# Performance work log

Measured on AMD Instinct MI355X. Metric: run time of the kernel, lower is better.

Reference implementation:

```python
import jax, jax.numpy as jnp
import numpy as np

M_DIM, Z_DIM, C = 256, 128, 32
N, L = 512, 384


def setup_inputs() -> dict:
    key = jax.random.key(0)
    ks = jax.random.split(key, 9)
    s = 1.0 / np.sqrt(M_DIM)
    return {
        "m": jax.random.normal(ks[0], (N, L, M_DIM), dtype=jnp.float32),
        "ln_gamma": jnp.ones((M_DIM,), jnp.float32),
        "ln_beta": jnp.zeros((M_DIM,), jnp.float32),
        "w1": jax.random.normal(ks[1], (M_DIM, C), jnp.float32) * s,
        "b1": jnp.zeros((C,), jnp.float32),
        "w2": jax.random.normal(ks[2], (M_DIM, C), jnp.float32) * s,
        "b2": jnp.zeros((C,), jnp.float32),
        "w3": jax.random.normal(ks[3], (C * C, Z_DIM), jnp.float32) * (1.0 / np.sqrt(C * C)),
        "b3": jnp.zeros((Z_DIM,), jnp.float32),
    }


def _layernorm(x, gamma, beta, eps=1e-5):
    mu = jnp.mean(x, axis=-1, keepdims=True)
    var = jnp.mean(jnp.square(x - mu), axis=-1, keepdims=True)
    return (x - mu) * jax.lax.rsqrt(var + eps) * gamma + beta


def reference(m, ln_gamma, ln_beta, w1, b1, w2, b2, w3, b3):
    n = m.shape[0]
    o = _layernorm(m, ln_gamma, ln_beta)          # (N, L, D)
    a = o @ w2 + b2                                # (N, L, C)  linear2
    b = o @ w1 + b1                                # (N, L, C)  linear1
    # mean over N of outer products: reassociated as a single contraction over n
    op = jnp.einsum('nia,njb->ijab', a, b) / n     # (L, L, C, C)
    ll = op.shape[0]
    z = op.reshape(ll, ll, -1) @ w3 + b3           # (L, L, Z)
    return z
```

## Files before the change

### kernel.cpp

```cpp
#include <hip/hip_runtime.h>
#include <hip/hip_bf16.h>
#include <stdint.h>

#define L_DIM 384
#define MD    256
#define CC    32
#define ZD    128
#define NB    512
#define K2    1024
#define MROWS 12288

typedef __attribute__((ext_vector_type(4)))  float f32x4;
typedef __attribute__((ext_vector_type(8)))  short bf16x8;

typedef __attribute__((address_space(1))) unsigned char* gcp;
typedef __attribute__((address_space(3))) unsigned char* lcp;

#define SBAR()  __builtin_amdgcn_s_barrier()
#define VMW(n)  asm volatile("s_waitcnt vmcnt(" #n ")" ::: "memory")
#define PRIO1() __builtin_amdgcn_s_setprio(1)
#define PRIO0() __builtin_amdgcn_s_setprio(0)

__device__ __forceinline__ unsigned short f2bf(float x) {
    union { float f; unsigned u; } v; v.f = x;
    unsigned r = v.u + 0x7fffu + ((v.u >> 16) & 1u);
    return (unsigned short)(r >> 16);
}

__device__ __forceinline__ uint2 pack4(unsigned short a, unsigned short b,
                                       unsigned short c, unsigned short d) {
    uint2 r; r.x = (unsigned)a | ((unsigned)b << 16);
    r.y = (unsigned)c | ((unsigned)d << 16); return r;
}

__global__ __launch_bounds__(256) void prep_kernel(
    const float* __restrict__ w1, const float* __restrict__ w2,
    const float* __restrict__ w3,
    unsigned short* __restrict__ w3frag, unsigned short* __restrict__ wfrag)
{
    int idx = blockIdx.x * 256 + threadIdx.x;
    if (idx < 131072) {
        int e = idx & 7, lane = (idx >> 3) & 63, zg = (idx >> 9) & 7, ks = idx >> 12;
        int k2p = ks * 32 + ((lane >> 4) << 3) + e;
        int wrow = (k2p & 31) * 32 + (k2p >> 5);
        int z  = zg * 16 + (lane & 15);
        w3frag[idx] = f2bf(w3[(size_t)wrow * ZD + z]);
    } else {
        int j = idx - 131072;
        int e = j & 7, lane = (j >> 3) & 63, nf = (j >> 9) & 3, ks = j >> 11;
        int c = nf * 16 + (lane & 15);
        int d = ks * 32 + ((lane >> 4) << 3) + e;
        float v = (c < CC) ? w2[d * CC + c] : w1[d * CC + (c - CC)];
        wfrag[j] = f2bf(v);
    }
}

__global__ __launch_bounds__(256, 4) void ln_proj_kernel(
    const float* __restrict__ mm, const float* __restrict__ gamma, const float* __restrict__ beta,
    const unsigned short* __restrict__ wfrag,
    const float* __restrict__ b1, const float* __restrict__ b2,
    unsigned short* __restrict__ At, unsigned short* __restrict__ Bt)
{
    __shared__ alignas(16) char o_b[32768];

    const int tid = threadIdx.x, wv = tid >> 6, lane = tid & 63;
    const int l0 = blockIdx.y * 2;
    const int n0 = blockIdx.x * 32;

    const int l_loc = wv >> 1;
    const int nbase = (wv & 1) << 4;
    const int l_g = l0 + l_loc;
    f32x4 g4 = *(const f32x4*)(gamma + lane * 4);
    f32x4 e4 = *(const f32x4*)(beta + lane * 4);

    #pragma unroll 4
    for (int r = 0; r < 16; ++r) {
        int row_loc = wv * 16 + r;
        int n_g = n0 + nbase + r;
        const float* src = mm + ((size_t)n_g * L_DIM + l_g) * MD + lane * 4;
        f32x4 x = *(const f32x4*)src;
        float s  = x[0] + x[1] + x[2] + x[3];
        float s2 = x[0]*x[0] + x[1]*x[1] + x[2]*x[2] + x[3]*x[3];
        #pragma unroll
        for (int off = 32; off > 0; off >>= 1) {
            s  += __shfl_xor(s,  off);
            s2 += __shfl_xor(s2, off);
        }
        float mu  = s * (1.0f / MD);
        float var = s2 * (1.0f / MD) - mu * mu;
        float rs  = rsqrtf(var + 1e-5f);
        unsigned short o0 = f2bf((x[0] - mu) * rs * g4[0] + e4[0]);
        unsigned short o1 = f2bf((x[1] - mu) * rs * g4[1] + e4[1]);
        unsigned short o2 = f2bf((x[2] - mu) * rs * g4[2] + e4[2]);
        unsigned short o3 = f2bf((x[3] - mu) * rs * g4[3] + e4[3]);
        *(uint2*)(o_b + row_loc * 512 + ((lane * 8) ^ ((row_loc & 7) << 4))) = pack4(o0, o1, o2, o3);
    }

    f32x4 acc[4] = {{0,0,0,0},{0,0,0,0},{0,0,0,0},{0,0,0,0}};
    const int lrow = lane & 15;
    const int kq16 = (lane >> 4) << 4;
    const int arow = wv * 16 + lrow;
    #pragma unroll
    for (int ks = 0; ks < 8; ++ks) {
        bf16x8 a = *(const bf16x8*)(o_b + arow * 512 + ((ks * 64 + kq16) ^ ((arow & 7) << 4)));
        #pragma unroll
        for (int nf = 0; nf < 4; ++nf) {
            bf16x8 b = *(const bf16x8*)(wfrag + (size_t)((ks * 4 + nf) * 64 + lane) * 8);
            acc[nf] = __builtin_amdgcn_mfma_f32_16x16x32_bf16(a, b, acc[nf], 0, 0, 0);
        }
    }

    const int rr0 = wv * 16 + ((lane >> 4) << 2);
    const int n_gw = n0 + (rr0 & 31);
    const int l_gw = l0 + (rr0 >> 5);
    #pragma unroll
    for (int nf = 0; nf < 4; ++nf) {
        int c = nf * 16 + lrow;
        float bias = (c < CC) ? b2[c] : b1[c - CC];
        unsigned short ob0 = f2bf(acc[nf][0] + bias);
        unsigned short ob1 = f2bf(acc[nf][1] + bias);
        unsigned short ob2 = f2bf(acc[nf][2] + bias);
        unsigned short ob3 = f2bf(acc[nf][3] + bias);
        unsigned short* dst = ((c < CC) ? At : Bt) + (size_t)(l_gw * CC + (c & 31)) * NB + n_gw;
        *(uint2*)dst = pack4(ob0, ob1, ob2, ob3);
    }
}

__global__ __launch_bounds__(512, 4) void opm_kernel(
    const unsigned short* __restrict__ At, const unsigned short* __restrict__ Bt,
    const unsigned short* __restrict__ w3frag, const float* __restrict__ b3,
    float* __restrict__ Z)
{
    __shared__ alignas(128) char smem[73728];
    const int tid = threadIdx.x, wv = tid >> 6, lane = tid & 63;

    const int lin = blockIdx.x;
    const int xcd = lin & 7, c = lin >> 3;
    const int i0 = (xcd * 12 + (c % 12)) * 128;
    const int j0 = (c / 12) * 256;

    const int lrow = lane & 15;
    const int wrB = (wv >> 2) * 64, wcB = (wv & 3) * 64;

    const int f0 = wv * 3;
    const int s_row = lane >> 2;
    const int s_kof = ((lane & 3) ^ (s_row & 3)) << 3;

    auto stage = [&](int t) {
        const int buf = t % 3;
        #pragma unroll
        for (int q = 0; q < 3; ++q) {
            int f = f0 + q;
            const unsigned short* g;
            char* l;
            if (f < 8) {
                g = At + (size_t)(i0 + f * 16 + s_row) * NB + t * 32 + s_kof;
                l = smem + buf * 8192 + f * 1024;
            } else {
                g = Bt + (size_t)(j0 + (f - 8) * 16 + s_row) * NB + t * 32 + s_kof;
                l = smem + 24576 + buf * 16384 + (f - 8) * 1024;
            }
            __builtin_amdgcn_global_load_lds((gcp)g, (lcp)l, 16, 0, 0);
        }
    };

    f32x4 acc[4][4] = {};
    const int rpos = ((lane >> 4) ^ (lane & 3)) << 4;

    auto TILE = [&](int t) {
        const char* ab = smem + (t % 3) * 8192;
        const char* bb = smem + 24576 + (t % 3) * 16384;
        bf16x8 av[4], bv[4];
        #pragma unroll
        for (int mf = 0; mf < 4; ++mf)
            av[mf] = *(const bf16x8*)(ab + (wrB + mf * 16 + lrow) * 64 + rpos);
        #pragma unroll
        for (int nf = 0; nf < 4; ++nf)
            bv[nf] = *(const bf16x8*)(bb + (wcB + nf * 16 + lrow) * 64 + rpos);
        PRIO1();
        #pragma unroll
        for (int mf = 0; mf < 4; ++mf)
            #pragma unroll
            for (int nf = 0; nf < 4; ++nf)
                acc[mf][nf] = __builtin_amdgcn_mfma_f32_16x16x32_bf16(
                    av[mf], bv[nf], acc[mf][nf], 0, 0, 0);
        PRIO0();
    };

    stage(0); stage(1);
    VMW(3);
    SBAR();

    #pragma unroll
    for (int t = 0; t < 16; ++t) {
        if (t < 14) stage(t + 2);
        TILE(t);
        if (t < 14)      { VMW(3); }
        else if (t == 14){ VMW(0); }
        SBAR();
    }

    char* const opb = smem;
    const int pf  = wv & 1;
    const int zgb = (wv >> 1) * 2;
    const int row0 = pf * 16 + lrow;
    const int lq = lane >> 4;

    auto ldW = [&](int ks, int zg) -> bf16x8 {
        return *(const bf16x8*)(w3frag + (size_t)((ks * 8 + zg) * 64 + lane) * 8);
    };
    auto ldP = [&](int row, int ks) -> bf16x8 {
        int g = ks * 4 + lq;
        int b = g >> 2, jj = g & 3;
        int inner = (b * 64 + jj * 16) ^ (((b >> 1) & 7) << 4) ^ ((row & 7) << 4);
        return *(const bf16x8*)(opb + row * 2048 + inner);
    };

    bf16x8 wA0 = ldW(0, zgb), wA1 = ldW(0, zgb + 1);

    const float scale = 1.0f / (float)NB;
    #pragma unroll
    for (int mf = 0; mf < 4; ++mf) {
        #pragma unroll
        for (int nf = 0; nf < 4; ++nf) {
            int col = wcB + nf * 16 + lrow;
            int bcol = col & 31;
            int row = wrB + mf * 16 + ((lane >> 4) << 2);
            int pl = ((row >> 5) << 3) | (col >> 5);
            int a0e = row & 31;
            int inner = (bcol * 64 + a0e * 2) ^ (((bcol >> 1) & 7) << 4) ^ ((pl & 7) << 4);
            *(uint2*)(opb + pl * 2048 + inner) =
                pack4(f2bf(acc[mf][nf][0] * scale), f2bf(acc[mf][nf][1] * scale),
                      f2bf(acc[mf][nf][2] * scale), f2bf(acc[mf][nf][3] * scale));
        }
    }
    __syncthreads();

    f32x4 acc2[2] = {};
    bf16x8 pA = ldP(row0, 0);
    for (int ks = 0; ks < 32; ++ks) {
        bf16x8 wN0 = {}, wN1 = {}, pN = {};
        if (ks + 1 < 32) {
            wN0 = ldW(ks + 1, zgb); wN1 = ldW(ks + 1, zgb + 1);
            pN  = ldP(row0, ks + 1);
        }
        PRIO1();
        acc2[0] = __builtin_amdgcn_mfma_f32_16x16x32_bf16(pA, wA0, acc2[0], 0, 0, 0);
        acc2[1] = __builtin_amdgcn_mfma_f32_16x16x32_bf16(pA, wA1, acc2[1], 0, 0, 0);
        PRIO0();
        wA0 = wN0; wA1 = wN1; pA = pN;
    }

    const int pq = (lane >> 4) << 2;
    #pragma unroll
    for (int zi = 0; zi < 2; ++zi) {
        int zc = (zgb + zi) * 16 + lrow;
        float bias = b3[zc];
        #pragma unroll
        for (int rr = 0; rr < 4; ++rr) {
            int pl = pf * 16 + pq + rr;
            int ii = (i0 >> 5) + (pl >> 3);
            int jj = (j0 >> 5) + (pl & 7);
            Z[((size_t)ii * L_DIM + jj) * ZD + zc] = acc2[zi][rr] + bias;
        }
    }
}

extern "C" void kernel_launch(void* const* d_in, const int* in_sizes, int n_in,
                              void* d_out, int out_size, void* d_ws, size_t ws_size,
                              hipStream_t stream)
{
    const float* mm    = (const float*)d_in[0];
    const float* gamma = (const float*)d_in[1];
    const float* beta  = (const float*)d_in[2];
    const float* w1    = (const float*)d_in[3];
    const float* b1    = (const float*)d_in[4];
    const float* w2    = (const float*)d_in[5];
    const float* b2    = (const float*)d_in[6];
    const float* w3    = (const float*)d_in[7];
    const float* b3    = (const float*)d_in[8];

    unsigned short* At     = (unsigned short*)d_ws;
    unsigned short* Bt     = At + (size_t)MROWS * NB;
    unsigned short* w3frag = Bt + (size_t)MROWS * NB;
    unsigned short* wfrag  = w3frag + 131072;

    prep_kernel<<<576, 256, 0, stream>>>(w1, w2, w3, w3frag, wfrag);
    ln_proj_kernel<<<dim3(16, 192), 256, 0, stream>>>(mm, gamma, beta, wfrag, b1, b2, At, Bt);
    opm_kernel<<<4608, 512, 0, stream>>>(At, Bt, w3frag, b3, (float*)d_out);
}
```

Measured before the change: 278.8 us.

## Switch OPM GEMM to 32x32 MFMA with B fragments prepacked in global memory

The first kernel now writes the B projection in an MFMA-fragment-ordered layout, so the outer-product kernel can load B operands straight from global memory into registers through a 4-deep register prefetch instead of staging them in LDS. Only A is staged, in 128-wide K chunks that are double-buffered, which cuts the number of barriers from 16 to a few and shrinks LDS use. The inner product uses 32x32x16 MFMAs with 2x2 accumulator tiles instead of 4x4 tiles of 16x16x32, and the epilogue scatter into the op buffer is adapted to the new accumulator layout. The risks are higher register pressure from the prefetched B fragments and more global traffic for B, since each wave reads its B fragments from cache directly.

```diff
diff --git a/kernel.cpp b/kernel.cpp
--- a/kernel.cpp
+++ b/kernel.cpp
@@ -11,6 +11,7 @@
 #define MROWS 12288
 
 typedef __attribute__((ext_vector_type(4)))  float f32x4;
+typedef __attribute__((ext_vector_type(16))) float f32x16;
 typedef __attribute__((ext_vector_type(8)))  short bf16x8;
 
 typedef __attribute__((address_space(1))) unsigned char* gcp;
@@ -117,12 +118,16 @@
     for (int nf = 0; nf < 4; ++nf) {
         int c = nf * 16 + lrow;
         float bias = (c < CC) ? b2[c] : b1[c - CC];
-        unsigned short ob0 = f2bf(acc[nf][0] + bias);
-        unsigned short ob1 = f2bf(acc[nf][1] + bias);
-        unsigned short ob2 = f2bf(acc[nf][2] + bias);
-        unsigned short ob3 = f2bf(acc[nf][3] + bias);
-        unsigned short* dst = ((c < CC) ? At : Bt) + (size_t)(l_gw * CC + (c & 31)) * NB + n_gw;
-        *(uint2*)dst = pack4(ob0, ob1, ob2, ob3);
+        uint2 pk = pack4(f2bf(acc[nf][0] + bias), f2bf(acc[nf][1] + bias),
+                         f2bf(acc[nf][2] + bias), f2bf(acc[nf][3] + bias));
+        if (c < CC) {
+            *(uint2*)(At + (size_t)(l_gw * CC + c) * NB + n_gw) = pk;
+        } else {
+            int c31 = c - CC;
+            size_t addr = (((size_t)l_gw * 32 + (n_gw >> 4)) * 64
+                           + c31 + (((n_gw >> 3) & 1) << 5)) * 8 + (n_gw & 7);
+            *(uint2*)(Bt + addr) = pk;
+        }
     }
 }
 
@@ -131,79 +136,71 @@
     const unsigned short* __restrict__ w3frag, const float* __restrict__ b3,
     float* __restrict__ Z)
 {
-    __shared__ alignas(128) char smem[73728];
+    __shared__ alignas(128) char smem[65536];
+    char* const Ab = smem;
+
     const int tid = threadIdx.x, wv = tid >> 6, lane = tid & 63;
 
     const int lin = blockIdx.x;
-    const int xcd = lin & 7, c = lin >> 3;
-    const int i0 = (xcd * 12 + (c % 12)) * 128;
-    const int j0 = (c / 12) * 256;
-
+    const int xcd = lin & 7, chunk = lin >> 3;
+    const int i0 = (xcd * 12 + (chunk % 12)) * 128;
+    const int j0 = (chunk / 12) * 256;
+
+    const int mrow = lane & 31;
+    const int kb16 = (lane >> 5) << 4;
+    const int swz  = (mrow & 15) << 4;
+    const int wr = (wv >> 2) * 64, wc = (wv & 3) * 64;
+    const int fb0 = (j0 + wc) >> 5;
+
+    auto stageA = [&](int t) {
+        char* base = Ab + (t & 1) * 32768;
+        #pragma unroll
+        for (int q = 0; q < 4; ++q) {
+            int r0 = wv * 16 + q * 4;
+            int row = r0 + (lane >> 4);
+            const unsigned short* gp = At + (size_t)(i0 + row) * NB + t * 128
+                                       + (((lane & 15) ^ (row & 15)) << 3);
+            __builtin_amdgcn_global_load_lds((gcp)gp, (lcp)(base + r0 * 256), 16, 0, 0);
+        }
+    };
+
+    auto loadBp = [&](bf16x8* dst, int s) {
+        #pragma unroll
+        for (int nf = 0; nf < 2; ++nf)
+            dst[nf] = *(const bf16x8*)(Bt + ((size_t)((fb0 + nf) * 32 + s) * 64 + lane) * 8);
+    };
+
+    f32x16 acc[2][2] = {};
+    bf16x8 bv[4][2];
+
+    stageA(0); stageA(1);
+    loadBp(bv[0], 0); loadBp(bv[1], 1); loadBp(bv[2], 2);
+    VMW(10);
+    SBAR();
+
+    #pragma unroll
+    for (int t = 0; t < 4; ++t) {
+        const char* ab = Ab + (t & 1) * 32768;
+        if (t >= 1 && t <= 2) stageA(t + 1);
+        #pragma unroll
+        for (int ks = 0; ks < 8; ++ks) {
+            const int s = t * 8 + ks;
+            bf16x8 av0 = *(const bf16x8*)(ab + (wr      + mrow) * 256 + ((ks * 32 + kb16) ^ swz));
+            bf16x8 av1 = *(const bf16x8*)(ab + (wr + 32 + mrow) * 256 + ((ks * 32 + kb16) ^ swz));
+            PRIO1();
+            acc[0][0] = __builtin_amdgcn_mfma_f32_32x32x16_bf16(av0, bv[s & 3][0], acc[0][0], 0, 0, 0);
+            acc[0][1] = __builtin_amdgcn_mfma_f32_32x32x16_bf16(av0, bv[s & 3][1], acc[0][1], 0, 0, 0);
+            acc[1][0] = __builtin_amdgcn_mfma_f32_32x32x16_bf16(av1, bv[s & 3][0], acc[1][0], 0, 0, 0);
+            acc[1][1] = __builtin_amdgcn_mfma_f32_32x32x16_bf16(av1, bv[s & 3][1], acc[1][1], 0, 0, 0);
+            PRIO0();
+            if (s + 3 < 32) loadBp(bv[(s + 3) & 3], s + 3);
+        }
+        if (t < 3) { VMW(6); SBAR(); }
+    }
+    __syncthreads();
+
+    char* const opb = smem;
     const int lrow = lane & 15;
-    const int wrB = (wv >> 2) * 64, wcB = (wv & 3) * 64;
-
-    const int f0 = wv * 3;
-    const int s_row = lane >> 2;
-    const int s_kof = ((lane & 3) ^ (s_row & 3)) << 3;
-
-    auto stage = [&](int t) {
-        const int buf = t % 3;
-        #pragma unroll
-        for (int q = 0; q < 3; ++q) {
-            int f = f0 + q;
-            const unsigned short* g;
-            char* l;
-            if (f < 8) {
-                g = At + (size_t)(i0 + f * 16 + s_row) * NB + t * 32 + s_kof;
-                l = smem + buf * 8192 + f * 1024;
-            } else {
-                g = Bt + (size_t)(j0 + (f - 8) * 16 + s_row) * NB + t * 32 + s_kof;
-                l = smem + 24576 + buf * 16384 + (f - 8) * 1024;
-            }
-            __builtin_amdgcn_global_load_lds((gcp)g, (lcp)l, 16, 0, 0);
-        }
-    };
-
-    f32x4 acc[4][4] = {};
-    const int rpos = ((lane >> 4) ^ (lane & 3)) << 4;
-
-    auto TILE = [&](int t) {
-        const char* ab = smem + (t % 3) * 8192;
-        const char* bb = smem + 24576 + (t % 3) * 16384;
-        bf16x8 av[4], bv[4];
-        #pragma unroll
-        for (int mf = 0; mf < 4; ++mf)
-            av[mf] = *(const bf16x8*)(ab + (wrB + mf * 16 + lrow) * 64 + rpos);
-        #pragma unroll
-        for (int nf = 0; nf < 4; ++nf)
-            bv[nf] = *(const bf16x8*)(bb + (wcB + nf * 16 + lrow) * 64 + rpos);
-        PRIO1();
-        #pragma unroll
-        for (int mf = 0; mf < 4; ++mf)
-            #pragma unroll
-            for (int nf = 0; nf < 4; ++nf)
-                acc[mf][nf] = __builtin_amdgcn_mfma_f32_16x16x32_bf16(
-                    av[mf], bv[nf], acc[mf][nf], 0, 0, 0);
-        PRIO0();
-    };
-
-    stage(0); stage(1);
-    VMW(3);
-    SBAR();
-
-    #pragma unroll
-    for (int t = 0; t < 16; ++t) {
-        if (t < 14) stage(t + 2);
-        TILE(t);
-        if (t < 14)      { VMW(3); }
-        else if (t == 14){ VMW(0); }
-        SBAR();
-    }
-
-    char* const opb = smem;
-    const int pf  = wv & 1;
-    const int zgb = (wv >> 1) * 2;
-    const int row0 = pf * 16 + lrow;
     const int lq = lane >> 4;
 
     auto ldW = [&](int ks, int zg) -> bf16x8 {
@@ -216,22 +213,29 @@
         return *(const bf16x8*)(opb + row * 2048 + inner);
     };
 
+    const int pf  = wv & 1;
+    const int zgb = (wv >> 1) * 2;
+    const int row0 = pf * 16 + lrow;
+
     bf16x8 wA0 = ldW(0, zgb), wA1 = ldW(0, zgb + 1);
 
     const float scale = 1.0f / (float)NB;
-    #pragma unroll
-    for (int mf = 0; mf < 4; ++mf) {
-        #pragma unroll
-        for (int nf = 0; nf < 4; ++nf) {
-            int col = wcB + nf * 16 + lrow;
-            int bcol = col & 31;
-            int row = wrB + mf * 16 + ((lane >> 4) << 2);
-            int pl = ((row >> 5) << 3) | (col >> 5);
-            int a0e = row & 31;
-            int inner = (bcol * 64 + a0e * 2) ^ (((bcol >> 1) & 7) << 4) ^ ((pl & 7) << 4);
-            *(uint2*)(opb + pl * 2048 + inner) =
-                pack4(f2bf(acc[mf][nf][0] * scale), f2bf(acc[mf][nf][1] * scale),
-                      f2bf(acc[mf][nf][2] * scale), f2bf(acc[mf][nf][3] * scale));
+    const int bcol = lane & 31;
+    const int hq4  = (lane >> 5) << 2;
+    #pragma unroll
+    for (int mf = 0; mf < 2; ++mf) {
+        #pragma unroll
+        for (int nf = 0; nf < 2; ++nf) {
+            int pl = (((wr + mf * 32) >> 5) << 3) | ((wc >> 5) + nf);
+            int swp = (((bcol >> 1) & 7) << 4) ^ ((pl & 7) << 4);
+            #pragma unroll
+            for (int q = 0; q < 4; ++q) {
+                int a0e = q * 8 + hq4;
+                int inner = (bcol * 64 + a0e * 2) ^ swp;
+                *(uint2*)(opb + pl * 2048 + inner) =
+                    pack4(f2bf(acc[mf][nf][4*q+0] * scale), f2bf(acc[mf][nf][4*q+1] * scale),
+                          f2bf(acc[mf][nf][4*q+2] * scale), f2bf(acc[mf][nf][4*q+3] * scale));
+            }
         }
     }
     __syncthreads();
```

New measurement: 279.4 us. Within noise of the previous version (+0.2%).
